# Kernel tuning notes

Hardware: AMD Instinct MI355X
Metric: run time of the kernel (lower is better)

Reference implementation:

```python
import jax, jax.numpy as jnp
import numpy as np

N_DRUGS = 10000
N_REL = 500
N_TARGETS = 20000
DIM = 128
B = 8192
K = 64
MAX_SCALE = 2.5   # self.scale (non-trainable)
MARGIN = 8.0


def _lorentz_random(key, n, d, std):
    # mimic Lorentz.random_normal: gaussian spatial part, time = sqrt(1+||x||^2)
    x = jax.random.normal(key, (n, d), dtype=jnp.float32) * std
    nar = x[:, 1:]
    time = jnp.sqrt(1.0 + jnp.sum(nar * nar, axis=-1, keepdims=True))
    return jnp.concatenate([time, nar], axis=-1)


def setup_inputs() -> dict:
    key = jax.random.key(0)
    ks = jax.random.split(key, 6)
    std = 1.0 / np.sqrt(DIM)
    drug_entity = _lorentz_random(ks[0], N_DRUGS, DIM, std)
    target_entity = _lorentz_random(ks[1], N_TARGETS, DIM, std)
    relation_bias = jnp.zeros((N_REL, DIM), dtype=jnp.float32)
    # kaiming_uniform_ on [n_rel, dim, dim]: fan_in = dim*dim, bound = sqrt(6/fan_in)
    bound = np.sqrt(6.0 / (DIM * DIM))
    relation_transform = jax.random.uniform(ks[2], (N_REL, DIM, DIM), dtype=jnp.float32,
                                            minval=-bound, maxval=bound)
    bias_head = jnp.zeros((N_DRUGS,), dtype=jnp.float32)
    bias_tail = jnp.zeros((N_TARGETS,), dtype=jnp.float32)
    u_idx = jax.random.randint(ks[3], (B,), 0, N_DRUGS, dtype=jnp.int32)
    r_idx = jax.random.randint(ks[4], (B,), 0, N_REL, dtype=jnp.int32)
    v_idx = jax.random.randint(ks[5], (B, K), 0, N_TARGETS, dtype=jnp.int32)
    return {"u_idx": u_idx, "r_idx": r_idx, "v_idx": v_idx,
            "drug_entity": drug_entity, "target_entity": target_entity,
            "relation_bias": relation_bias, "relation_transform": relation_transform,
            "bias_head": bias_head, "bias_tail": bias_tail}


def reference(u_idx, r_idx, v_idx, drug_entity, target_entity,
              relation_bias, relation_transform, bias_head, bias_tail):
    head = drug_entity[u_idx]                # [B, d] gather
    W = relation_transform[r_idx]            # [B, d, d] gather
    rb = relation_bias[r_idx]                 # [B, d] gather
    # lorentz_linear4decoder: x = head @ W^T (per sample)
    x = jnp.einsum('bd,bed->be', head, W)     # [B, d]
    time = jax.nn.sigmoid(x[:, :1]) * MAX_SCALE + 1.1   # [B, 1], from pre-bias x
    x = x + rb                                 # bias added after time
    nar = x[:, 1:]                             # [B, d-1]
    nar = nar / jnp.sqrt(jnp.sum(nar * nar, axis=-1, keepdims=True) / (time * time - 1.0))
    tail = target_entity[v_idx]               # [B, K, d] gather
    # cinner: spatial dot minus time product
    cin = jnp.einsum('bd,bkd->bk', nar, tail[..., 1:]) - time * tail[..., 0]  # [B, K]
    neg_dist = MARGIN + 2.0 * cin
    return neg_dist + bias_head[u_idx][:, None] + bias_tail[v_idx]
```

## Files before the change

### kernel.cpp

```cpp
#include <hip/hip_runtime.h>
#include <math.h>

#define N_B 8192
#define N_K 64
#define DD  128
#define N_RELC 500

__global__ __launch_bounds__(1024) void sort_kernel(const int* __restrict__ r_idx,
                                                    const int* __restrict__ u_idx,
                                                    int* __restrict__ perm,
                                                    int* __restrict__ uperm,
                                                    int* __restrict__ offs)
{
    __shared__ int hist[512];
    __shared__ int scan[512];
    __shared__ int cur[512];
    const int t = threadIdx.x;
    if (t < 512) hist[t] = 0;
    __syncthreads();

    int rv[8];
#pragma unroll
    for (int k = 0; k < 8; ++k) {
        rv[k] = r_idx[t + 1024 * k];
        atomicAdd(&hist[rv[k]], 1);
    }
    __syncthreads();
    if (t < 512) scan[t] = hist[t];
    __syncthreads();
    for (int off = 1; off < 512; off <<= 1) {
        int v = 0;
        if (t < 512 && t >= off) v = scan[t - off];
        __syncthreads();
        if (t < 512) scan[t] += v;
        __syncthreads();
    }
    if (t < 512) {
        const int excl = scan[t] - hist[t];
        cur[t] = excl;
        if (t <= N_RELC) offs[t] = excl;
    }
    __syncthreads();
#pragma unroll
    for (int k = 0; k < 8; ++k) {
        const int b   = t + 1024 * k;
        const int pos = atomicAdd(&cur[rv[k]], 1);
        perm[pos]  = b;
        uperm[pos] = u_idx[b];
    }
}

__global__ __launch_bounds__(256) void hybo_main(
    const int* __restrict__ v_idx,
    const float* __restrict__ drug_entity, const float* __restrict__ target_entity,
    const float* __restrict__ relation_bias, const float* __restrict__ relation_transform,
    const float* __restrict__ bias_head, const float* __restrict__ bias_tail,
    const int* __restrict__ perm, const int* __restrict__ uperm,
    const int* __restrict__ offs,
    float* __restrict__ out)
{
    const int bid = blockIdx.x;
    const int x   = bid & 7;
    const int i   = bid >> 3;
    const int rc  = i >> 4;
    const int s   = i & 15;
    const int r   = (rc << 3) | x;
    if (r >= N_RELC) return;

    const int beg = offs[r];
    const int n   = offs[r + 1] - beg;
    if (n <= s) return;

    const int tid  = threadIdx.x;
    const int lane = tid & 63;
    const int wave = tid >> 6;
    const int q    = lane & 15;
    const int g    = lane >> 4;

    __shared__ float x_lds[DD];
    __shared__ float y_lds[DD];
    __shared__ float red_lds[4];

    const float rbv = (tid < DD) ? relation_bias[r * DD + tid] : 0.0f;
    const float* Wb = relation_transform + (size_t)r * (DD * DD);

    for (int p = s; p < n; p += 16) {
        const int b = perm[beg + p];
        const int u = uperm[beg + p];

        int vi[4];
#pragma unroll
        for (int ii = 0; ii < 4; ++ii)
            vi[ii] = v_idx[(size_t)b * N_K + wave * 16 + ii * 4 + g];

        const float4 h0 = *reinterpret_cast<const float4*>(drug_entity + (size_t)u * DD + 8 * q);
        const float4 h1 = *reinterpret_cast<const float4*>(drug_entity + (size_t)u * DD + 8 * q + 4);
        const float  bh = bias_head[u];

        float4 wv[16];
#pragma unroll
        for (int ii = 0; ii < 8; ++ii) {
            const float* row = Wb + (wave * 32 + ii * 4 + g) * DD + 8 * q;
            wv[2 * ii]     = *reinterpret_cast<const float4*>(row);
            wv[2 * ii + 1] = *reinterpret_cast<const float4*>(row + 4);
        }
#pragma unroll
        for (int ii = 0; ii < 8; ++ii) {
            float p2;
            p2 = wv[2 * ii].x * h0.x;
            p2 = fmaf(wv[2 * ii].y,     h0.y, p2);
            p2 = fmaf(wv[2 * ii].z,     h0.z, p2);
            p2 = fmaf(wv[2 * ii].w,     h0.w, p2);
            p2 = fmaf(wv[2 * ii + 1].x, h1.x, p2);
            p2 = fmaf(wv[2 * ii + 1].y, h1.y, p2);
            p2 = fmaf(wv[2 * ii + 1].z, h1.z, p2);
            p2 = fmaf(wv[2 * ii + 1].w, h1.w, p2);
            p2 += __shfl_xor(p2, 1, 64);
            p2 += __shfl_xor(p2, 2, 64);
            p2 += __shfl_xor(p2, 4, 64);
            p2 += __shfl_xor(p2, 8, 64);
            if (q == 0) x_lds[wave * 32 + ii * 4 + g] = p2;
        }

        float4 t0[4], t1[4];
        float  bt[4];
#pragma unroll
        for (int ii = 0; ii < 4; ++ii) {
            const float* trow = target_entity + (size_t)vi[ii] * DD + 8 * q;
            t0[ii] = *reinterpret_cast<const float4*>(trow);
            t1[ii] = *reinterpret_cast<const float4*>(trow + 4);
            bt[ii] = bias_tail[vi[ii]];
        }

        __syncthreads();

        const float x0 = x_lds[0];
        float xv = 0.0f, sq = 0.0f;
        if (tid < DD) {
            xv = x_lds[tid] + rbv;
            y_lds[tid] = xv;
            if (tid > 0) sq = xv * xv;
        }
        float ps = sq;
#pragma unroll
        for (int m = 32; m >= 1; m >>= 1) ps += __shfl_xor(ps, m, 64);
        if (lane == 0) red_lds[wave] = ps;
        __syncthreads();

        const float timev = 2.5f / (1.0f + expf(-x0)) + 1.1f;
        const float ssum  = red_lds[0] + red_lds[1] + red_lds[2] + red_lds[3];
        const float f     = sqrtf((timev * timev - 1.0f) / ssum);

        float4 ya = *reinterpret_cast<const float4*>(&y_lds[8 * q]);
        float4 yb = *reinterpret_cast<const float4*>(&y_lds[8 * q + 4]);
        ya.x = (q == 0) ? -timev : ya.x * f;
        ya.y *= f; ya.z *= f; ya.w *= f;
        yb.x *= f; yb.y *= f; yb.z *= f; yb.w *= f;

#pragma unroll
        for (int ii = 0; ii < 4; ++ii) {
            float p2;
            p2 = t0[ii].x * ya.x;
            p2 = fmaf(t0[ii].y, ya.y, p2);
            p2 = fmaf(t0[ii].z, ya.z, p2);
            p2 = fmaf(t0[ii].w, ya.w, p2);
            p2 = fmaf(t1[ii].x, yb.x, p2);
            p2 = fmaf(t1[ii].y, yb.y, p2);
            p2 = fmaf(t1[ii].z, yb.z, p2);
            p2 = fmaf(t1[ii].w, yb.w, p2);
            p2 += __shfl_xor(p2, 1, 64);
            p2 += __shfl_xor(p2, 2, 64);
            p2 += __shfl_xor(p2, 4, 64);
            p2 += __shfl_xor(p2, 8, 64);
            if (q == 0)
                out[(size_t)b * N_K + wave * 16 + ii * 4 + g] = fmaf(2.0f, p2, 8.0f) + bh + bt[ii];
        }
    }
}

extern "C" void kernel_launch(void* const* d_in, const int* in_sizes, int n_in,
                              void* d_out, int out_size, void* d_ws, size_t ws_size,
                              hipStream_t stream) {
    const int*   u_idx  = (const int*)d_in[0];
    const int*   r_idx  = (const int*)d_in[1];
    const int*   v_idx  = (const int*)d_in[2];
    const float* drug   = (const float*)d_in[3];
    const float* targ   = (const float*)d_in[4];
    const float* rbias  = (const float*)d_in[5];
    const float* rtrans = (const float*)d_in[6];
    const float* bhead  = (const float*)d_in[7];
    const float* btail  = (const float*)d_in[8];
    float* out = (float*)d_out;

    int* perm  = (int*)d_ws;
    int* uperm = perm + N_B;
    int* offs  = uperm + N_B;

    hipLaunchKernelGGL(sort_kernel, dim3(1), dim3(1024), 0, stream,
                       r_idx, u_idx, perm, uperm, offs);
    hipLaunchKernelGGL(hybo_main, dim3(8064), dim3(256), 0, stream,
                       v_idx, drug, targ, rbias, rtrans, bhead, btail,
                       perm, uperm, offs, out);
}
```

Before: 180.9 us.

## Process four samples per block, reusing each W row load across them

Each block now handles four samples of the same relation at once. A W row is loaded once and dotted with four head vectors, so relation-matrix traffic per sample drops to a quarter. Each wave then owns one sample's normalisation and all 64 tail dots, and target-row loads are double-buffered across the four groups of 16. The grid shrinks to 8 slices per relation and launch bounds request 4 blocks per CU. In exchange register pressure rises, and fewer blocks are launched, which could lower parallelism for relations with few samples.

```diff
diff --git a/kernel.cpp b/kernel.cpp
--- a/kernel.cpp
+++ b/kernel.cpp
@@ -5,6 +5,7 @@
 #define N_K 64
 #define DD  128
 #define N_RELC 500
+#define SLICES 8
 
 __global__ __launch_bounds__(1024) void sort_kernel(const int* __restrict__ r_idx,
                                                     const int* __restrict__ u_idx,
@@ -50,7 +51,28 @@
     }
 }
 
-__global__ __launch_bounds__(256) void hybo_main(
+__device__ __forceinline__ float dot8(const float4 a0, const float4 a1,
+                                      const float4 b0, const float4 b1) {
+    float p = a0.x * b0.x;
+    p = fmaf(a0.y, b0.y, p);
+    p = fmaf(a0.z, b0.z, p);
+    p = fmaf(a0.w, b0.w, p);
+    p = fmaf(a1.x, b1.x, p);
+    p = fmaf(a1.y, b1.y, p);
+    p = fmaf(a1.z, b1.z, p);
+    p = fmaf(a1.w, b1.w, p);
+    return p;
+}
+
+__device__ __forceinline__ float red16(float p) {
+    p += __shfl_xor(p, 1, 64);
+    p += __shfl_xor(p, 2, 64);
+    p += __shfl_xor(p, 4, 64);
+    p += __shfl_xor(p, 8, 64);
+    return p;
+}
+
+__global__ __launch_bounds__(256, 4) void hybo_main(
     const int* __restrict__ v_idx,
     const float* __restrict__ drug_entity, const float* __restrict__ target_entity,
     const float* __restrict__ relation_bias, const float* __restrict__ relation_transform,
@@ -62,119 +84,130 @@
     const int bid = blockIdx.x;
     const int x   = bid & 7;
     const int i   = bid >> 3;
-    const int rc  = i >> 4;
-    const int s   = i & 15;
+    const int rc  = i >> 3;
+    const int s   = i & 7;
     const int r   = (rc << 3) | x;
     if (r >= N_RELC) return;
 
     const int beg = offs[r];
     const int n   = offs[r + 1] - beg;
-    if (n <= s) return;
+    if (s * 4 >= n) return;
 
     const int tid  = threadIdx.x;
     const int lane = tid & 63;
-    const int wave = tid >> 6;
+    const int w    = tid >> 6;
     const int q    = lane & 15;
     const int g    = lane >> 4;
 
-    __shared__ float x_lds[DD];
-    __shared__ float y_lds[DD];
-    __shared__ float red_lds[4];
-
-    const float rbv = (tid < DD) ? relation_bias[r * DD + tid] : 0.0f;
-    const float* Wb = relation_transform + (size_t)r * (DD * DD);
-
-    for (int p = s; p < n; p += 16) {
-        const int b = perm[beg + p];
-        const int u = uperm[beg + p];
-
-        int vi[4];
-#pragma unroll
-        for (int ii = 0; ii < 4; ++ii)
-            vi[ii] = v_idx[(size_t)b * N_K + wave * 16 + ii * 4 + g];
-
-        const float4 h0 = *reinterpret_cast<const float4*>(drug_entity + (size_t)u * DD + 8 * q);
-        const float4 h1 = *reinterpret_cast<const float4*>(drug_entity + (size_t)u * DD + 8 * q + 4);
-        const float  bh = bias_head[u];
-
-        float4 wv[16];
+    __shared__ float x_lds[4][DD];
+
+    const float* Wb  = relation_transform + (size_t)r * (DD * DD);
+    const float4 rb0 = *reinterpret_cast<const float4*>(relation_bias + r * DD + 8 * q);
+    const float4 rb1 = *reinterpret_cast<const float4*>(relation_bias + r * DD + 8 * q + 4);
+
+    for (int p0 = s * 4; p0 < n; p0 += SLICES * 4) {
+        if (p0 != s * 4) __syncthreads();
+
+        int uu[4];
+#pragma unroll
+        for (int j = 0; j < 4; ++j) {
+            int p = p0 + j; if (p >= n) p = n - 1;
+            uu[j] = uperm[beg + p];
+        }
+        const bool live = (p0 + w < n);
+        const int  pw   = live ? (p0 + w) : (n - 1);
+        const int  bw   = perm[beg + pw];
+        const float bh  = bias_head[uperm[beg + pw]];
+
+        const int* vb = v_idx + (size_t)bw * N_K;
+        int vi[16];
+#pragma unroll
+        for (int t = 0; t < 16; ++t) vi[t] = vb[t * 4 + g];
+
+        float4 h0[4], h1[4];
+#pragma unroll
+        for (int j = 0; j < 4; ++j) {
+            const float* hp = drug_entity + (size_t)uu[j] * DD + 8 * q;
+            h0[j] = *reinterpret_cast<const float4*>(hp);
+            h1[j] = *reinterpret_cast<const float4*>(hp + 4);
+        }
+
 #pragma unroll
         for (int ii = 0; ii < 8; ++ii) {
-            const float* row = Wb + (wave * 32 + ii * 4 + g) * DD + 8 * q;
-            wv[2 * ii]     = *reinterpret_cast<const float4*>(row);
-            wv[2 * ii + 1] = *reinterpret_cast<const float4*>(row + 4);
-        }
-#pragma unroll
-        for (int ii = 0; ii < 8; ++ii) {
-            float p2;
-            p2 = wv[2 * ii].x * h0.x;
-            p2 = fmaf(wv[2 * ii].y,     h0.y, p2);
-            p2 = fmaf(wv[2 * ii].z,     h0.z, p2);
-            p2 = fmaf(wv[2 * ii].w,     h0.w, p2);
-            p2 = fmaf(wv[2 * ii + 1].x, h1.x, p2);
-            p2 = fmaf(wv[2 * ii + 1].y, h1.y, p2);
-            p2 = fmaf(wv[2 * ii + 1].z, h1.z, p2);
-            p2 = fmaf(wv[2 * ii + 1].w, h1.w, p2);
-            p2 += __shfl_xor(p2, 1, 64);
-            p2 += __shfl_xor(p2, 2, 64);
-            p2 += __shfl_xor(p2, 4, 64);
-            p2 += __shfl_xor(p2, 8, 64);
-            if (q == 0) x_lds[wave * 32 + ii * 4 + g] = p2;
-        }
-
-        float4 t0[4], t1[4];
-        float  bt[4];
-#pragma unroll
-        for (int ii = 0; ii < 4; ++ii) {
-            const float* trow = target_entity + (size_t)vi[ii] * DD + 8 * q;
-            t0[ii] = *reinterpret_cast<const float4*>(trow);
-            t1[ii] = *reinterpret_cast<const float4*>(trow + 4);
-            bt[ii] = bias_tail[vi[ii]];
+            const int e = w * 32 + ii * 4 + g;
+            const float* row = Wb + e * DD + 8 * q;
+            const float4 wv0 = *reinterpret_cast<const float4*>(row);
+            const float4 wv1 = *reinterpret_cast<const float4*>(row + 4);
+            float pa = dot8(wv0, wv1, h0[0], h1[0]);
+            float pb = dot8(wv0, wv1, h0[1], h1[1]);
+            float pc = dot8(wv0, wv1, h0[2], h1[2]);
+            float pd = dot8(wv0, wv1, h0[3], h1[3]);
+            pa = red16(pa); pb = red16(pb); pc = red16(pc); pd = red16(pd);
+            if (q == 0) {
+                x_lds[0][e] = pa; x_lds[1][e] = pb;
+                x_lds[2][e] = pc; x_lds[3][e] = pd;
+            }
+        }
+
+        float4 t0A[4], t1A[4]; float btA[4];
+#pragma unroll
+        for (int ii2 = 0; ii2 < 4; ++ii2) {
+            const float* trow = target_entity + (size_t)vi[ii2] * DD + 8 * q;
+            t0A[ii2] = *reinterpret_cast<const float4*>(trow);
+            t1A[ii2] = *reinterpret_cast<const float4*>(trow + 4);
+            btA[ii2] = bias_tail[vi[ii2]];
         }
 
         __syncthreads();
 
-        const float x0 = x_lds[0];
-        float xv = 0.0f, sq = 0.0f;
-        if (tid < DD) {
-            xv = x_lds[tid] + rbv;
-            y_lds[tid] = xv;
-            if (tid > 0) sq = xv * xv;
-        }
-        float ps = sq;
-#pragma unroll
-        for (int m = 32; m >= 1; m >>= 1) ps += __shfl_xor(ps, m, 64);
-        if (lane == 0) red_lds[wave] = ps;
-        __syncthreads();
-
-        const float timev = 2.5f / (1.0f + expf(-x0)) + 1.1f;
-        const float ssum  = red_lds[0] + red_lds[1] + red_lds[2] + red_lds[3];
+        const float x0v = x_lds[w][0];
+        float4 xa = *reinterpret_cast<const float4*>(&x_lds[w][8 * q]);
+        float4 xb = *reinterpret_cast<const float4*>(&x_lds[w][8 * q + 4]);
+        xa.x += rb0.x; xa.y += rb0.y; xa.z += rb0.z; xa.w += rb0.w;
+        xb.x += rb1.x; xb.y += rb1.y; xb.z += rb1.z; xb.w += rb1.w;
+        float sq = xa.y * xa.y + xa.z * xa.z + xa.w * xa.w
+                 + xb.x * xb.x + xb.y * xb.y + xb.z * xb.z + xb.w * xb.w;
+        if (q != 0) sq = fmaf(xa.x, xa.x, sq);
+        const float ssum  = red16(sq);
+        const float timev = 2.5f / (1.0f + expf(-x0v)) + 1.1f;
         const float f     = sqrtf((timev * timev - 1.0f) / ssum);
-
-        float4 ya = *reinterpret_cast<const float4*>(&y_lds[8 * q]);
-        float4 yb = *reinterpret_cast<const float4*>(&y_lds[8 * q + 4]);
-        ya.x = (q == 0) ? -timev : ya.x * f;
-        ya.y *= f; ya.z *= f; ya.w *= f;
-        yb.x *= f; yb.y *= f; yb.z *= f; yb.w *= f;
-
-#pragma unroll
-        for (int ii = 0; ii < 4; ++ii) {
-            float p2;
-            p2 = t0[ii].x * ya.x;
-            p2 = fmaf(t0[ii].y, ya.y, p2);
-            p2 = fmaf(t0[ii].z, ya.z, p2);
-            p2 = fmaf(t0[ii].w, ya.w, p2);
-            p2 = fmaf(t1[ii].x, yb.x, p2);
-            p2 = fmaf(t1[ii].y, yb.y, p2);
-            p2 = fmaf(t1[ii].z, yb.z, p2);
-            p2 = fmaf(t1[ii].w, yb.w, p2);
-            p2 += __shfl_xor(p2, 1, 64);
-            p2 += __shfl_xor(p2, 2, 64);
-            p2 += __shfl_xor(p2, 4, 64);
-            p2 += __shfl_xor(p2, 8, 64);
-            if (q == 0)
-                out[(size_t)b * N_K + wave * 16 + ii * 4 + g] = fmaf(2.0f, p2, 8.0f) + bh + bt[ii];
-        }
+        float4 ya, yb;
+        ya.x = (q == 0) ? -timev : xa.x * f;
+        ya.y = xa.y * f; ya.z = xa.z * f; ya.w = xa.w * f;
+        yb.x = xb.x * f; yb.y = xb.y * f; yb.z = xb.z * f; yb.w = xb.w * f;
+
+#define PREFETCH(T0, T1, BT, BLK)                                                   \
+        {                                                                           \
+            _Pragma("unroll")                                                       \
+            for (int ii2 = 0; ii2 < 4; ++ii2) {                                     \
+                const float* trow = target_entity + (size_t)vi[(BLK)*4+ii2] * DD + 8*q; \
+                T0[ii2] = *reinterpret_cast<const float4*>(trow);                   \
+                T1[ii2] = *reinterpret_cast<const float4*>(trow + 4);               \
+                BT[ii2] = bias_tail[vi[(BLK)*4+ii2]];                               \
+            }                                                                       \
+        }
+#define COMPUTE(T0, T1, BT, BLK)                                                    \
+        {                                                                           \
+            _Pragma("unroll")                                                       \
+            for (int ii2 = 0; ii2 < 4; ++ii2) {                                     \
+                float pd2 = dot8(T0[ii2], T1[ii2], ya, yb);                         \
+                pd2 = red16(pd2);                                                   \
+                if (live && q == 0)                                                 \
+                    out[(size_t)bw * N_K + (BLK)*16 + ii2*4 + g] =                  \
+                        fmaf(2.0f, pd2, 8.0f) + bh + BT[ii2];                       \
+            }                                                                       \
+        }
+
+        float4 t0B[4], t1B[4]; float btB[4];
+        PREFETCH(t0B, t1B, btB, 1)
+        COMPUTE(t0A, t1A, btA, 0)
+        PREFETCH(t0A, t1A, btA, 2)
+        COMPUTE(t0B, t1B, btB, 1)
+        PREFETCH(t0B, t1B, btB, 3)
+        COMPUTE(t0A, t1A, btA, 2)
+        COMPUTE(t0B, t1B, btB, 3)
+#undef PREFETCH
+#undef COMPUTE
     }
 }
 
@@ -198,7 +231,7 @@
 
     hipLaunchKernelGGL(sort_kernel, dim3(1), dim3(1024), 0, stream,
                        r_idx, u_idx, perm, uperm, offs);
-    hipLaunchKernelGGL(hybo_main, dim3(8064), dim3(256), 0, stream,
+    hipLaunchKernelGGL(hybo_main, dim3(8 * 63 * SLICES), dim3(256), 0, stream,
                        v_idx, drug, targ, rbias, rtrans, bhead, btail,
                        perm, uperm, offs, out);
 }
```

Result: slower. 256.1 us (+41.6%).
